# Kernel optimization log

Hardware: AMD Instinct MI355X
Metric: run time of the kernel (lower is better)

Reference implementation:

```python
import jax, jax.numpy as jnp
import numpy as np

S, B, TD = 1024, 2, 138
D, H, Dh, L, F = 1024, 16, 64, 8, 2048
EPS = 1e-5


def setup_inputs() -> dict:
    key = jax.random.key(0)
    ks = jax.random.split(key, 32)
    std = 0.02

    def w(k, shape):
        return (jax.random.normal(k, shape, jnp.float32) * std)

    return {
        'tokens': jax.random.normal(ks[0], (S, B, TD), jnp.float32),
        'Win': w(ks[1], (D, TD)), 'bin_': jnp.zeros((D,), jnp.float32),
        'pos_emb': w(ks[2], (S, D)),
        'Wq': w(ks[3], (L, D, D)), 'bq': jnp.zeros((L, D), jnp.float32),
        'Wk': w(ks[4], (L, D, D)), 'bk': jnp.zeros((L, D), jnp.float32),
        'Wv': w(ks[5], (L, D, D)), 'bv': jnp.zeros((L, D), jnp.float32),
        'Wo': w(ks[6], (L, D, D)), 'bo': jnp.zeros((L, D), jnp.float32),
        'W1': w(ks[7], (L, F, D)), 'b1': jnp.zeros((L, F), jnp.float32),
        'W2': w(ks[8], (L, D, F)), 'b2': jnp.zeros((L, D), jnp.float32),
        'g1': jnp.ones((L, D), jnp.float32), 'be1': jnp.zeros((L, D), jnp.float32),
        'g2': jnp.ones((L, D), jnp.float32), 'be2': jnp.zeros((L, D), jnp.float32),
        'Wh': w(ks[9], (1, D)), 'bh': jnp.zeros((1,), jnp.float32),
    }


def _ln(x, g, b):
    mu = jnp.mean(x, axis=-1, keepdims=True)
    var = jnp.mean(jnp.square(x - mu), axis=-1, keepdims=True)
    return (x - mu) * jax.lax.rsqrt(var + EPS) * g + b


def _rope_tables(seq_len):
    inv_freq = 1.0 / (10000.0 ** (jnp.arange(0, Dh, 2, dtype=jnp.float32) / Dh))
    ang = jnp.arange(seq_len, dtype=jnp.float32)[:, None] * inv_freq  # (S, Dh/2)
    cos = jnp.repeat(jnp.cos(ang), 2, axis=-1)  # (S, Dh) interleaved
    sin = jnp.repeat(jnp.sin(ang), 2, axis=-1)
    return cos, sin


def _apply_rope(x, cos, sin):
    # x: (B, H, S, Dh); rotate_every_two: pairs (x0, x1) -> (-x1, x0)
    rot = jnp.stack([-x[..., 1::2], x[..., 0::2]], axis=-1).reshape(x.shape)
    return x * cos + rot * sin


def reference(tokens, Win, bin_, pos_emb, Wq, bq, Wk, bk, Wv, bv, Wo, bo,
              W1, b1, W2, b2, g1, be1, g2, be2, Wh, bh):
    s = tokens.shape[0]
    x = jnp.einsum('sbt,dt->sbd', tokens, Win) + bin_ + pos_emb[:s, None, :]
    cos, sin = _rope_tables(s)
    causal = jnp.tril(jnp.ones((s, s), dtype=bool))
    scale = 1.0 / np.sqrt(Dh)

    def to_heads(y):  # (S,B,D) -> (B,H,S,Dh)
        return jnp.transpose(y.reshape(s, -1, H, Dh), (1, 2, 0, 3))

    def layer(x, p):
        wq, bq_, wk, bk_, wv, bv_, wo, bo_, w1, b1_, w2, b2_, g1_, be1_, g2_, be2_ = p
        qh = _apply_rope(to_heads(jnp.einsum('sbd,ed->sbe', x, wq) + bq_), cos, sin)
        kh = _apply_rope(to_heads(jnp.einsum('sbd,ed->sbe', x, wk) + bk_), cos, sin)
        vh = to_heads(jnp.einsum('sbd,ed->sbe', x, wv) + bv_)
        scores = jnp.einsum('bhqd,bhkd->bhqk', qh, kh) * scale
        scores = jnp.where(causal, scores, -jnp.inf)
        attn = jax.nn.softmax(scores, axis=-1)
        o = jnp.einsum('bhqk,bhkd->bhqd', attn, vh)  # (B,H,S,Dh)
        o = jnp.transpose(o, (2, 0, 1, 3)).reshape(s, -1, D)
        attn_out = jnp.einsum('sbd,ed->sbe', o, wo) + bo_
        src2 = _ln(x + attn_out, g1_, be1_)
        ff = jnp.einsum('sbf,df->sbd', jax.nn.relu(jnp.einsum('sbd,fd->sbf', src2, w1) + b1_), w2) + b2_
        return _ln(src2 + ff, g2_, be2_), None

    params = (Wq, bq, Wk, bk, Wv, bv, Wo, bo, W1, b1, W2, b2, g1, be1, g2, be2)
    x, _ = jax.lax.scan(layer, x, params)
    return jnp.einsum('sbd,od->sbo', x, Wh) + bh  # (S, B, 1)
```

## Files before the change

### kernel.cpp

```cpp
#include <hip/hip_runtime.h>
#include <hip/hip_bf16.h>

typedef __hip_bfloat16 bf16;
typedef float f32x4 __attribute__((ext_vector_type(4)));
typedef float f32x16 __attribute__((ext_vector_type(16)));
typedef short s16x8 __attribute__((ext_vector_type(8)));
typedef int i32x4 __attribute__((ext_vector_type(4)));

#define S_LEN 1024
#define BATCH 2
#define TDIM 138
#define KPAD 160
#define DMOD 1024
#define NHEAD 16
#define DHEAD 64
#define NLAYER 8
#define FDIM 2048
#define MROWS 2048
static const size_t DD_ = (size_t)DMOD * DMOD;
static const size_t FD_ = (size_t)FDIM * DMOD;

__device__ __forceinline__ void load_lds16(const bf16* g, bf16* l) {
  __builtin_amdgcn_global_load_lds((const __attribute__((address_space(1))) void*)g,
                                   (__attribute__((address_space(3))) void*)l, 16, 0, 0);
}

__device__ __forceinline__ unsigned pack2(float a, float b) {
  unsigned x = __builtin_bit_cast(unsigned short, __float2bfloat16(a));
  unsigned y = __builtin_bit_cast(unsigned short, __float2bfloat16(b));
  return x | (y << 16);
}

__device__ __forceinline__ int chunk_start(int c) {
  return c == 0 ? 0 : (c == 1 ? 32 : (c == 2 ? 56 : 72));
}

__global__ __launch_bounds__(256) void f2b_layer(
    const float4* __restrict__ Wq, const float4* __restrict__ Wk,
    const float4* __restrict__ Wv, const float4* __restrict__ Wo,
    const float4* __restrict__ W1, const float4* __restrict__ W2,
    ushort4* __restrict__ dst) {
  int i = blockIdx.x * 256 + threadIdx.x;
  const int DD4 = (int)(DD_ / 4), FD4 = (int)(FD_ / 4);
  if (i >= 4 * DD4 + 2 * FD4) return;
  const float4* src; int off;
  if (i < 3 * DD4) { int w = i / DD4; off = i - w * DD4; src = w == 0 ? Wq : (w == 1 ? Wk : Wv); }
  else if (i < 4 * DD4) { src = Wo; off = i - 3 * DD4; }
  else if (i < 4 * DD4 + FD4) { src = W1; off = i - 4 * DD4; }
  else { src = W2; off = i - 4 * DD4 - FD4; }
  float4 v = src[off];
  ushort4 o;
  o.x = __builtin_bit_cast(unsigned short, __float2bfloat16(v.x));
  o.y = __builtin_bit_cast(unsigned short, __float2bfloat16(v.y));
  o.z = __builtin_bit_cast(unsigned short, __float2bfloat16(v.z));
  o.w = __builtin_bit_cast(unsigned short, __float2bfloat16(v.w));
  dst[i] = o;
}

__global__ __launch_bounds__(256) void pad_cvt(const float* __restrict__ in,
                                               bf16* __restrict__ out, int R) {
  int i = blockIdx.x * 256 + threadIdx.x;
  if (i >= R * KPAD) return;
  int r = i / KPAD, t = i - r * KPAD;
  out[i] = __float2bfloat16(t < TDIM ? in[r * TDIM + t] : 0.0f);
}

__global__ __launch_bounds__(256) void rope_table(float2* __restrict__ t) {
  int idx = blockIdx.x * 256 + threadIdx.x;
  if (idx >= S_LEN * 32) return;
  int s = idx >> 5, i = idx & 31;
  float freq = __expf(-(float)i * (2.0f / (float)DHEAD) * 9.210340371976184f);
  float sn, cs;
  sincosf((float)s * freq, &sn, &cs);
  t[idx] = make_float2(cs, sn);
}

template<int TN, int EPI>
__global__ __launch_bounds__(256) void gemm128(
    const bf16* __restrict__ A, const bf16* __restrict__ W,
    const float* __restrict__ b0p, const float* __restrict__ b1p, const float* __restrict__ b2p,
    const float2* __restrict__ rope2, float* __restrict__ Cf,
    bf16* __restrict__ Cb0, bf16* __restrict__ Cb1, bf16* __restrict__ Cb2,
    int N, int K, int nbx) {
  constexpr int NJ = TN / 32;
  constexpr int ASZ = 128 * 32, BSZ = TN * 32;
  __shared__ bf16 As[2 * ASZ];
  __shared__ bf16 Bs[2 * BSZ];
  int nwg = gridDim.x, bid = blockIdx.x;
  int wg = (bid & 7) * (nwg >> 3) + (bid >> 3);
  int bx = wg % nbx, by = wg / nbx;
  int bn = bx * TN, bm = by * 128;
  int tid = threadIdx.x, lane = tid & 63, w = tid >> 6;
  int lo = lane & 15, hi = lane >> 4;
  int wr = (w >> 1) * 64, wc = (w & 1) * (TN / 2);
  f32x4 acc[4][NJ] = {};

  int srow = tid >> 2, sseg = tid & 3;
  const bf16* gA = A + (size_t)(bm + srow) * K + sseg * 8;
  const bf16* gB = W + (size_t)(bn + srow) * K + sseg * 8;
  bf16* lA0 = As + srow * 32 + sseg * 8;
  bf16* lB0 = Bs + srow * 32 + sseg * 8;

  auto STAGE = [&](int k0, int b) {
    load_lds16(gA + k0, lA0 + b * ASZ);
    load_lds16(gA + (size_t)64 * K + k0, lA0 + b * ASZ + 64 * 32);
    load_lds16(gB + k0, lB0 + b * BSZ);
    if constexpr (TN == 128) load_lds16(gB + (size_t)64 * K + k0, lB0 + b * BSZ + 64 * 32);
  };

  int nt = K / 32;
  STAGE(0, 0);
  __syncthreads();
  int cur = 0;
  for (int t = 0; t < nt; t++) {
    if (t + 1 < nt) STAGE((t + 1) * 32, cur ^ 1);
    const bf16* Ab = As + cur * ASZ;
    const bf16* Bb = Bs + cur * BSZ;
    s16x8 af[4], bfr[NJ];
#pragma unroll
    for (int mi = 0; mi < 4; mi++) af[mi] = *(const s16x8*)(Ab + (wr + mi * 16 + lo) * 32 + hi * 8);
#pragma unroll
    for (int nj = 0; nj < NJ; nj++) bfr[nj] = *(const s16x8*)(Bb + (wc + nj * 16 + lo) * 32 + hi * 8);
#pragma unroll
    for (int mi = 0; mi < 4; mi++)
#pragma unroll
      for (int nj = 0; nj < NJ; nj++)
        acc[mi][nj] = __builtin_amdgcn_mfma_f32_16x16x32_bf16(af[mi], bfr[nj], acc[mi][nj], 0, 0, 0);
    __syncthreads();
    cur ^= 1;
  }

#pragma unroll
  for (int mi = 0; mi < 4; mi++)
#pragma unroll
    for (int nj = 0; nj < NJ; nj++)
#pragma unroll
      for (int r = 0; r < 4; r++) {
        int m = bm + wr + mi * 16 + hi * 4 + r;
        int n = bn + wc + nj * 16 + lo;
        float v = acc[mi][nj][r];
        if constexpr (EPI == 0) {
          int which = n >> 10;
          int d = n & 1023, h = d >> 6, dh = d & 63;
          int s = m >> 1, bb = m & 1;
          const float* bp = which == 0 ? b0p : (which == 1 ? b1p : b2p);
          v += bp[d];
          if (which < 2) {
            float pv = __shfl_xor(v, 1);
            float2 cn = rope2[s * 32 + (dh >> 1)];
            float o = (dh & 1) ? (v * cn.x + pv * cn.y) : (v * cn.x - pv * cn.y);
            bf16* dst = which == 0 ? Cb0 : Cb1;
            dst[(((size_t)(bb * NHEAD + h)) * S_LEN + s) * DHEAD + dh] = __float2bfloat16(o);
          } else {
            Cb2[(((size_t)(bb * NHEAD + h)) * DHEAD + dh) * S_LEN + s] = __float2bfloat16(v);
          }
        } else if constexpr (EPI == 1) {
          Cf[(size_t)m * N + n] = v + b0p[n];
        } else if constexpr (EPI == 2) {
          Cb0[(size_t)m * N + n] = __float2bfloat16(fmaxf(v + b0p[n], 0.0f));
        } else {
          float v2 = v + b0p[n] + b1p[(size_t)(m >> 1) * DMOD + n];
          Cf[(size_t)m * N + n] = v2;
          Cb0[(size_t)m * N + n] = __float2bfloat16(v2);
        }
      }
}

__global__ __launch_bounds__(256) void flash_part(const bf16* __restrict__ Q,
    const bf16* __restrict__ K, const bf16* __restrict__ Vt,
    float* __restrict__ pO, float* __restrict__ pML) {
  int bid = blockIdx.x;
  int xcd = bid & 7, idx = bid >> 3;
  int bh = xcd * 4 + idx / 20;
  int w = threadIdx.x >> 6, lane = threadIdx.x & 63;
  int widx = (idx % 20) * 4 + w;
  int c = widx < 32 ? 0 : (widx < 56 ? 1 : (widx < 72 ? 2 : 3));
  int qt = widx - chunk_start(c) + 8 * c;
  int l31 = lane & 31, hi1 = lane >> 5;
  int q0 = qt * 32, kc0 = c * 256;
  int kend = min(kc0 + 256, q0 + 32);
  int nkt = (kend - kc0 + 31) >> 5;

  const size_t qkb = (size_t)bh * S_LEN * DHEAD;
  const bf16* qp = Q + qkb + (size_t)(q0 + l31) * DHEAD + hi1 * 8;
  s16x8 bq0 = *(const s16x8*)(qp);
  s16x8 bq1 = *(const s16x8*)(qp + 16);
  s16x8 bq2 = *(const s16x8*)(qp + 32);
  s16x8 bq3 = *(const s16x8*)(qp + 48);
  const bf16* kB = K + qkb;
  const bf16* vB = Vt + qkb;
  f32x16 accO0 = {}, accO1 = {};
  float mv = -INFINITY, lv = 0.0f;
  const float SC = 0.18033688011112042f;

  auto loadTile = [&](int kc, s16x8& k0, s16x8& k1, s16x8& k2, s16x8& k3,
                      s16x8& v0, s16x8& v1, s16x8& v2, s16x8& v3) {
    const bf16* kp = kB + (size_t)(kc + l31) * DHEAD + hi1 * 8;
    k0 = *(const s16x8*)(kp);
    k1 = *(const s16x8*)(kp + 16);
    k2 = *(const s16x8*)(kp + 32);
    k3 = *(const s16x8*)(kp + 48);
    const bf16* vp = vB + (size_t)l31 * S_LEN + kc + hi1 * 8;
    v0 = *(const s16x8*)(vp);
    v1 = *(const s16x8*)(vp + 16);
    v2 = *(const s16x8*)(vp + (size_t)32 * S_LEN);
    v3 = *(const s16x8*)(vp + (size_t)32 * S_LEN + 16);
  };

  auto computeTile = [&](int kc, s16x8 ka0, s16x8 ka1, s16x8 ka2, s16x8 ka3,
                         s16x8 va00, s16x8 va01, s16x8 va10, s16x8 va11) {
    f32x16 st = {};
    st = __builtin_amdgcn_mfma_f32_32x32x16_bf16(ka0, bq0, st, 0, 0, 0);
    st = __builtin_amdgcn_mfma_f32_32x32x16_bf16(ka1, bq1, st, 0, 0, 0);
    st = __builtin_amdgcn_mfma_f32_32x32x16_bf16(ka2, bq2, st, 0, 0, 0);
    st = __builtin_amdgcn_mfma_f32_32x32x16_bf16(ka3, bq3, st, 0, 0, 0);

    bool diag = (kc >= q0);
    float pmax = -INFINITY;
#pragma unroll
    for (int j = 0; j < 16; j++) {
      float s = st[j] * SC;
      if (diag) {
        int krow = kc + (j & 3) + 8 * (j >> 2) + 4 * hi1;
        if (krow > q0 + l31) s = -INFINITY;
      }
      st[j] = s;
      pmax = fmaxf(pmax, s);
    }
    pmax = fmaxf(pmax, __shfl_xor(pmax, 32));
    float mnew = fmaxf(mv, pmax);
    float fs = exp2f(mv - mnew);
    float sum = 0.0f;
#pragma unroll
    for (int j = 0; j < 16; j++) {
      float e = exp2f(st[j] - mnew);
      st[j] = e;
      sum += e;
    }
    sum += __shfl_xor(sum, 32);
    lv = lv * fs + sum;
    mv = mnew;
    accO0 = accO0 * fs;
    accO1 = accO1 * fs;

    unsigned w0 = pack2(st[0], st[1]),   w1 = pack2(st[2], st[3]);
    unsigned w2 = pack2(st[4], st[5]),   w3 = pack2(st[6], st[7]);
    unsigned w4 = pack2(st[8], st[9]),   w5 = pack2(st[10], st[11]);
    unsigned w6 = pack2(st[12], st[13]), w7 = pack2(st[14], st[15]);
    unsigned xw0 = (unsigned)__shfl_xor((int)w0, 32), xw1 = (unsigned)__shfl_xor((int)w1, 32);
    unsigned xw2 = (unsigned)__shfl_xor((int)w2, 32), xw3 = (unsigned)__shfl_xor((int)w3, 32);
    unsigned xw4 = (unsigned)__shfl_xor((int)w4, 32), xw5 = (unsigned)__shfl_xor((int)w5, 32);
    unsigned xw6 = (unsigned)__shfl_xor((int)w6, 32), xw7 = (unsigned)__shfl_xor((int)w7, 32);
    bool hb = (hi1 != 0);
    i32x4 f0, f1;
    f0.x = (int)(hb ? xw2 : w0); f0.y = (int)(hb ? xw3 : w1);
    f0.z = (int)(hb ? w2 : xw0); f0.w = (int)(hb ? w3 : xw1);
    f1.x = (int)(hb ? xw6 : w4); f1.y = (int)(hb ? xw7 : w5);
    f1.z = (int)(hb ? w6 : xw4); f1.w = (int)(hb ? w7 : xw5);
    s16x8 pf0 = __builtin_bit_cast(s16x8, f0);
    s16x8 pf1 = __builtin_bit_cast(s16x8, f1);
    accO0 = __builtin_amdgcn_mfma_f32_32x32x16_bf16(va00, pf0, accO0, 0, 0, 0);
    accO0 = __builtin_amdgcn_mfma_f32_32x32x16_bf16(va01, pf1, accO0, 0, 0, 0);
    accO1 = __builtin_amdgcn_mfma_f32_32x32x16_bf16(va10, pf0, accO1, 0, 0, 0);
    accO1 = __builtin_amdgcn_mfma_f32_32x32x16_bf16(va11, pf1, accO1, 0, 0, 0);
  };

  s16x8 A0, A1, A2, A3, A4, A5, A6, A7;
  s16x8 B0, B1, B2, B3, B4, B5, B6, B7;
  loadTile(kc0, A0, A1, A2, A3, A4, A5, A6, A7);
  for (int kt = 0; kt < nkt; kt += 2) {
    if (kt + 1 < nkt) loadTile(kc0 + (kt + 1) * 32, B0, B1, B2, B3, B4, B5, B6, B7);
    computeTile(kc0 + kt * 32, A0, A1, A2, A3, A4, A5, A6, A7);
    if (kt + 1 < nkt) {
      if (kt + 2 < nkt) loadTile(kc0 + (kt + 2) * 32, A0, A1, A2, A3, A4, A5, A6, A7);
      computeTile(kc0 + (kt + 1) * 32, B0, B1, B2, B3, B4, B5, B6, B7);
    }
  }

  int pbase = bh * 80 + widx;
  float* po = pO + (size_t)pbase * 2048 + l31 * 64 + 4 * hi1;
#pragma unroll
  for (int jj = 0; jj < 4; jj++) {
    f32x4 v0 = {accO0[4 * jj], accO0[4 * jj + 1], accO0[4 * jj + 2], accO0[4 * jj + 3]};
    f32x4 v1 = {accO1[4 * jj], accO1[4 * jj + 1], accO1[4 * jj + 2], accO1[4 * jj + 3]};
    *(f32x4*)(po + 8 * jj) = v0;
    *(f32x4*)(po + 32 + 8 * jj) = v1;
  }
  if (hi1 == 0) {
    pML[pbase * 64 + l31] = mv;
    pML[pbase * 64 + 32 + l31] = lv;
  }
}

__global__ __launch_bounds__(256) void flash_merge(const float* __restrict__ pO,
    const float* __restrict__ pML, bf16* __restrict__ O) {
  int bid = blockIdx.x;
  int xcd = bid & 7, idx = bid >> 3;
  int bh = xcd * 4 + idx / 32, qt = idx % 32;
  int b = bh >> 4, h = bh & 15;
  int nch = (qt >> 3) + 1;
  int t = threadIdx.x;
  int dh = t & 63, r0 = t >> 6;
  int ibase = bh * 80;
#pragma unroll
  for (int j = 0; j < 8; j++) {
    int row = j * 4 + r0;
    float ms = -INFINITY;
    for (int cc = 0; cc < nch; cc++) {
      int wi = chunk_start(cc) + qt - 8 * cc;
      ms = fmaxf(ms, pML[(ibase + wi) * 64 + row]);
    }
    float l = 0.0f, o = 0.0f;
    for (int cc = 0; cc < nch; cc++) {
      int wi = chunk_start(cc) + qt - 8 * cc;
      float wgt = exp2f(pML[(ibase + wi) * 64 + row] - ms);
      l += wgt * pML[(ibase + wi) * 64 + 32 + row];
      o += wgt * pO[(size_t)(ibase + wi) * 2048 + row * 64 + dh];
    }
    int q = qt * 32 + row;
    O[((size_t)q * BATCH + b) * DMOD + h * DHEAD + dh] = __float2bfloat16(o / l);
  }
}

__global__ __launch_bounds__(256) void ln_kernel(const float* __restrict__ a,
    const float* __restrict__ r, const float* __restrict__ g,
    const float* __restrict__ be, float* __restrict__ outf, bf16* __restrict__ outb) {
  int m = blockIdx.x;
  int tid = threadIdx.x;
  float vals[4];
  float s1 = 0.f, s2 = 0.f;
  for (int j = 0; j < 4; j++) {
    int d = tid + j * 256;
    float v = a[(size_t)m * DMOD + d] + r[(size_t)m * DMOD + d];
    vals[j] = v; s1 += v; s2 += v * v;
  }
  __shared__ float red[8];
  for (int d = 1; d < 64; d <<= 1) { s1 += __shfl_xor(s1, d); s2 += __shfl_xor(s2, d); }
  int w = tid >> 6, lane = tid & 63;
  if (lane == 0) { red[w] = s1; red[4 + w] = s2; }
  __syncthreads();
  s1 = red[0] + red[1] + red[2] + red[3];
  s2 = red[4] + red[5] + red[6] + red[7];
  float mean = s1 * (1.0f / DMOD);
  float var = s2 * (1.0f / DMOD) - mean * mean;
  float rstd = rsqrtf(var + 1e-5f);
  for (int j = 0; j < 4; j++) {
    int d = tid + j * 256;
    float o = (vals[j] - mean) * rstd * g[d] + be[d];
    outf[(size_t)m * DMOD + d] = o;
    outb[(size_t)m * DMOD + d] = __float2bfloat16(o);
  }
}

__global__ __launch_bounds__(256) void head_kernel(const float* __restrict__ x,
    const float* __restrict__ Wh, const float* __restrict__ bh, float* __restrict__ out) {
  int m = blockIdx.x * 4 + (threadIdx.x >> 6);
  int lane = threadIdx.x & 63;
  float s = 0.f;
  for (int j = 0; j < 16; j++) {
    int d = lane + j * 64;
    s += x[(size_t)m * DMOD + d] * Wh[d];
  }
  for (int d = 1; d < 64; d <<= 1) s += __shfl_xor(s, d);
  if (lane == 0) out[m] = s + bh[0];
}

extern "C" void kernel_launch(void* const* d_in, const int* in_sizes, int n_in,
                              void* d_out, int out_size, void* d_ws, size_t ws_size,
                              hipStream_t stream) {
  (void)in_sizes; (void)n_in; (void)out_size; (void)ws_size;
  const float* tokens = (const float*)d_in[0];
  const float* Win    = (const float*)d_in[1];
  const float* binp   = (const float*)d_in[2];
  const float* pos    = (const float*)d_in[3];
  const float* Wq     = (const float*)d_in[4];
  const float* bq     = (const float*)d_in[5];
  const float* Wk     = (const float*)d_in[6];
  const float* bk     = (const float*)d_in[7];
  const float* Wv     = (const float*)d_in[8];
  const float* bv     = (const float*)d_in[9];
  const float* Wo     = (const float*)d_in[10];
  const float* bo     = (const float*)d_in[11];
  const float* W1     = (const float*)d_in[12];
  const float* b1     = (const float*)d_in[13];
  const float* W2     = (const float*)d_in[14];
  const float* b2     = (const float*)d_in[15];
  const float* g1     = (const float*)d_in[16];
  const float* be1    = (const float*)d_in[17];
  const float* g2     = (const float*)d_in[18];
  const float* be2    = (const float*)d_in[19];
  const float* Wh     = (const float*)d_in[20];
  const float* bhp    = (const float*)d_in[21];
  float* out = (float*)d_out;

  char* p = (char*)d_ws;
  auto alloc = [&](size_t bytes) { char* r = p; p += (bytes + 255) & ~(size_t)255; return r; };
  float* xf   = (float*)alloc((size_t)MROWS * DMOD * 4);
  bf16*  xb   = (bf16*) alloc((size_t)MROWS * DMOD * 2);
  float* x2f  = (float*)alloc((size_t)MROWS * DMOD * 4);
  bf16*  x2b  = (bf16*) alloc((size_t)MROWS * DMOD * 2);
  float* tmpf = (float*)alloc((size_t)MROWS * DMOD * 4);
  bf16*  qb   = (bf16*) alloc((size_t)MROWS * DMOD * 2);
  bf16*  kb   = (bf16*) alloc((size_t)MROWS * DMOD * 2);
  bf16*  vt   = (bf16*) alloc((size_t)MROWS * DMOD * 2);
  bf16*  ob   = (bf16*) alloc((size_t)MROWS * DMOD * 2);
  bf16*  hb   = (bf16*) alloc((size_t)MROWS * FDIM * 2);
  bf16*  wb   = (bf16*) alloc((4 * DD_ + 2 * FD_) * 2);
  bf16*  tokb = (bf16*) alloc((size_t)MROWS * KPAD * 2);
  bf16*  winb = (bf16*) alloc((size_t)DMOD * KPAD * 2);
  float2* rope2 = (float2*)alloc((size_t)S_LEN * 32 * 8);
  float* pO   = (float*)alloc((size_t)32 * 80 * 2048 * 4);
  float* pML  = (float*)alloc((size_t)32 * 80 * 64 * 4);

  rope_table<<<(S_LEN * 32 + 255) / 256, 256, 0, stream>>>(rope2);
  pad_cvt<<<(MROWS * KPAD + 255) / 256, 256, 0, stream>>>(tokens, tokb, MROWS);
  pad_cvt<<<(DMOD * KPAD + 255) / 256, 256, 0, stream>>>(Win, winb, DMOD);
  gemm128<128, 3><<<128, 256, 0, stream>>>(
      tokb, winb, binp, pos, nullptr, nullptr,
      xf, xb, nullptr, nullptr, DMOD, KPAD, 8);

  const int nW4 = (int)((4 * DD_ + 2 * FD_) / 4);

  for (int l = 0; l < NLAYER; l++) {
    f2b_layer<<<(nW4 + 255) / 256, 256, 0, stream>>>(
        (const float4*)(Wq + l * DD_), (const float4*)(Wk + l * DD_),
        (const float4*)(Wv + l * DD_), (const float4*)(Wo + l * DD_),
        (const float4*)(W1 + l * FD_), (const float4*)(W2 + l * FD_), (ushort4*)wb);

    gemm128<128, 0><<<384, 256, 0, stream>>>(
        xb, wb, bq + l * DMOD, bk + l * DMOD, bv + l * DMOD, rope2,
        nullptr, qb, kb, vt, 3 * DMOD, DMOD, 24);

    flash_part<<<640, 256, 0, stream>>>(qb, kb, vt, pO, pML);
    flash_merge<<<1024, 256, 0, stream>>>(pO, pML, ob);

    gemm128<64, 1><<<256, 256, 0, stream>>>(
        ob, wb + 3 * DD_, bo + l * DMOD, nullptr, nullptr, nullptr,
        tmpf, nullptr, nullptr, nullptr, DMOD, DMOD, 16);

    ln_kernel<<<MROWS, 256, 0, stream>>>(xf, tmpf, g1 + l * DMOD, be1 + l * DMOD, x2f, x2b);

    gemm128<128, 2><<<256, 256, 0, stream>>>(
        x2b, wb + 4 * DD_, b1 + l * FDIM, nullptr, nullptr, nullptr,
        nullptr, hb, nullptr, nullptr, FDIM, DMOD, 16);

    gemm128<64, 1><<<256, 256, 0, stream>>>(
        hb, wb + 4 * DD_ + FD_, b2 + l * DMOD, nullptr, nullptr, nullptr,
        tmpf, nullptr, nullptr, nullptr, DMOD, FDIM, 16);

    ln_kernel<<<MROWS, 256, 0, stream>>>(x2f, tmpf, g2 + l * DMOD, be2 + l * DMOD, xf, xb);
  }

  head_kernel<<<MROWS / 4, 256, 0, stream>>>(xf, Wh, bhp, out);
}
```

Baseline: 1.598 ms.

## Use 64x128 GEMM tiles with split-K for N=1024 projections, reduced in LayerNorm

Replaces the 128xTN GEMM tile with a 64x128 tile, doubling the workgroup count for every projection so more of the GPU's compute units stay busy. The Wo and W2 GEMMs (N=1024) also split K in two, writing two partial fp32 buffers that the LayerNorm kernel sums along with the residual. This targets underutilisation from the low workgroup counts of the previous launches. In exchange it adds extra fp32 partial writes and reads plus lower per-tile data reuse.

```diff
diff --git a/kernel.cpp b/kernel.cpp
--- a/kernel.cpp
+++ b/kernel.cpp
@@ -75,40 +75,42 @@
   t[idx] = make_float2(cs, sn);
 }
 
-template<int TN, int EPI>
-__global__ __launch_bounds__(256) void gemm128(
+template<int EPI, int SPLITK>
+__global__ __launch_bounds__(256) void gemm64(
     const bf16* __restrict__ A, const bf16* __restrict__ W,
     const float* __restrict__ b0p, const float* __restrict__ b1p, const float* __restrict__ b2p,
     const float2* __restrict__ rope2, float* __restrict__ Cf,
     bf16* __restrict__ Cb0, bf16* __restrict__ Cb1, bf16* __restrict__ Cb2,
-    int N, int K, int nbx) {
-  constexpr int NJ = TN / 32;
-  constexpr int ASZ = 128 * 32, BSZ = TN * 32;
+    int N, int K, int nby) {
+  constexpr int ASZ = 64 * 32, BSZ = 128 * 32;
   __shared__ bf16 As[2 * ASZ];
   __shared__ bf16 Bs[2 * BSZ];
   int nwg = gridDim.x, bid = blockIdx.x;
   int wg = (bid & 7) * (nwg >> 3) + (bid >> 3);
-  int bx = wg % nbx, by = wg / nbx;
-  int bn = bx * TN, bm = by * 128;
+  int nbx = N >> 7;
+  int by = wg % nby, bx2 = wg / nby;
+  int kh = 0, bx = bx2;
+  if constexpr (SPLITK == 2) { bx = bx2 % nbx; kh = bx2 / nbx; }
+  int bn = bx * 128, bm = by * 64;
+  int Kh = K / SPLITK, koff = kh * Kh;
   int tid = threadIdx.x, lane = tid & 63, w = tid >> 6;
   int lo = lane & 15, hi = lane >> 4;
-  int wr = (w >> 1) * 64, wc = (w & 1) * (TN / 2);
-  f32x4 acc[4][NJ] = {};
-
-  int srow = tid >> 2, sseg = tid & 3;
-  const bf16* gA = A + (size_t)(bm + srow) * K + sseg * 8;
-  const bf16* gB = W + (size_t)(bn + srow) * K + sseg * 8;
-  bf16* lA0 = As + srow * 32 + sseg * 8;
-  bf16* lB0 = Bs + srow * 32 + sseg * 8;
+  int wr = (w >> 1) * 32, wc = (w & 1) * 64;
+  f32x4 acc[2][4] = {};
+
+  int srow = tid >> 2, sseg = (tid & 3) * 8;
+  const bf16* gA = A + (size_t)(bm + srow) * K + koff + sseg;
+  const bf16* gB = W + (size_t)(bn + srow) * K + koff + sseg;
+  bf16* lA = As + srow * 32 + sseg;
+  bf16* lB = Bs + srow * 32 + sseg;
 
   auto STAGE = [&](int k0, int b) {
-    load_lds16(gA + k0, lA0 + b * ASZ);
-    load_lds16(gA + (size_t)64 * K + k0, lA0 + b * ASZ + 64 * 32);
-    load_lds16(gB + k0, lB0 + b * BSZ);
-    if constexpr (TN == 128) load_lds16(gB + (size_t)64 * K + k0, lB0 + b * BSZ + 64 * 32);
+    load_lds16(gA + k0, lA + b * ASZ);
+    load_lds16(gB + k0, lB + b * BSZ);
+    load_lds16(gB + (size_t)64 * K + k0, lB + b * BSZ + 64 * 32);
   };
 
-  int nt = K / 32;
+  int nt = Kh / 32;
   STAGE(0, 0);
   __syncthreads();
   int cur = 0;
@@ -116,24 +118,24 @@
     if (t + 1 < nt) STAGE((t + 1) * 32, cur ^ 1);
     const bf16* Ab = As + cur * ASZ;
     const bf16* Bb = Bs + cur * BSZ;
-    s16x8 af[4], bfr[NJ];
-#pragma unroll
-    for (int mi = 0; mi < 4; mi++) af[mi] = *(const s16x8*)(Ab + (wr + mi * 16 + lo) * 32 + hi * 8);
-#pragma unroll
-    for (int nj = 0; nj < NJ; nj++) bfr[nj] = *(const s16x8*)(Bb + (wc + nj * 16 + lo) * 32 + hi * 8);
-#pragma unroll
-    for (int mi = 0; mi < 4; mi++)
-#pragma unroll
-      for (int nj = 0; nj < NJ; nj++)
+    s16x8 af[2], bfr[4];
+#pragma unroll
+    for (int mi = 0; mi < 2; mi++) af[mi] = *(const s16x8*)(Ab + (wr + mi * 16 + lo) * 32 + hi * 8);
+#pragma unroll
+    for (int nj = 0; nj < 4; nj++) bfr[nj] = *(const s16x8*)(Bb + (wc + nj * 16 + lo) * 32 + hi * 8);
+#pragma unroll
+    for (int mi = 0; mi < 2; mi++)
+#pragma unroll
+      for (int nj = 0; nj < 4; nj++)
         acc[mi][nj] = __builtin_amdgcn_mfma_f32_16x16x32_bf16(af[mi], bfr[nj], acc[mi][nj], 0, 0, 0);
     __syncthreads();
     cur ^= 1;
   }
 
 #pragma unroll
-  for (int mi = 0; mi < 4; mi++)
-#pragma unroll
-    for (int nj = 0; nj < NJ; nj++)
+  for (int mi = 0; mi < 2; mi++)
+#pragma unroll
+    for (int nj = 0; nj < 4; nj++)
 #pragma unroll
       for (int r = 0; r < 4; r++) {
         int m = bm + wr + mi * 16 + hi * 4 + r;
@@ -155,7 +157,8 @@
             Cb2[(((size_t)(bb * NHEAD + h)) * DHEAD + dh) * S_LEN + s] = __float2bfloat16(v);
           }
         } else if constexpr (EPI == 1) {
-          Cf[(size_t)m * N + n] = v + b0p[n];
+          if (SPLITK == 1 || kh == 0) v += b0p[n];
+          Cf[((size_t)kh * MROWS + m) * N + n] = v;
         } else if constexpr (EPI == 2) {
           Cb0[(size_t)m * N + n] = __float2bfloat16(fmaxf(v + b0p[n], 0.0f));
         } else {
@@ -323,15 +326,17 @@
 }
 
 __global__ __launch_bounds__(256) void ln_kernel(const float* __restrict__ a,
-    const float* __restrict__ r, const float* __restrict__ g,
-    const float* __restrict__ be, float* __restrict__ outf, bf16* __restrict__ outb) {
+    const float* __restrict__ r0, const float* __restrict__ r1,
+    const float* __restrict__ g, const float* __restrict__ be,
+    float* __restrict__ outf, bf16* __restrict__ outb) {
   int m = blockIdx.x;
   int tid = threadIdx.x;
   float vals[4];
   float s1 = 0.f, s2 = 0.f;
   for (int j = 0; j < 4; j++) {
     int d = tid + j * 256;
-    float v = a[(size_t)m * DMOD + d] + r[(size_t)m * DMOD + d];
+    size_t i = (size_t)m * DMOD + d;
+    float v = a[i] + r0[i] + r1[i];
     vals[j] = v; s1 += v; s2 += v * v;
   }
   __shared__ float red[8];
@@ -399,7 +404,7 @@
   bf16*  xb   = (bf16*) alloc((size_t)MROWS * DMOD * 2);
   float* x2f  = (float*)alloc((size_t)MROWS * DMOD * 4);
   bf16*  x2b  = (bf16*) alloc((size_t)MROWS * DMOD * 2);
-  float* tmpf = (float*)alloc((size_t)MROWS * DMOD * 4);
+  float* tmpf = (float*)alloc((size_t)2 * MROWS * DMOD * 4);
   bf16*  qb   = (bf16*) alloc((size_t)MROWS * DMOD * 2);
   bf16*  kb   = (bf16*) alloc((size_t)MROWS * DMOD * 2);
   bf16*  vt   = (bf16*) alloc((size_t)MROWS * DMOD * 2);
@@ -415,9 +420,9 @@
   rope_table<<<(S_LEN * 32 + 255) / 256, 256, 0, stream>>>(rope2);
   pad_cvt<<<(MROWS * KPAD + 255) / 256, 256, 0, stream>>>(tokens, tokb, MROWS);
   pad_cvt<<<(DMOD * KPAD + 255) / 256, 256, 0, stream>>>(Win, winb, DMOD);
-  gemm128<128, 3><<<128, 256, 0, stream>>>(
+  gemm64<3, 1><<<256, 256, 0, stream>>>(
       tokb, winb, binp, pos, nullptr, nullptr,
-      xf, xb, nullptr, nullptr, DMOD, KPAD, 8);
+      xf, xb, nullptr, nullptr, DMOD, KPAD, 32);
 
   const int nW4 = (int)((4 * DD_ + 2 * FD_) / 4);
 
@@ -427,28 +432,30 @@
         (const float4*)(Wv + l * DD_), (const float4*)(Wo + l * DD_),
         (const float4*)(W1 + l * FD_), (const float4*)(W2 + l * FD_), (ushort4*)wb);
 
-    gemm128<128, 0><<<384, 256, 0, stream>>>(
+    gemm64<0, 1><<<768, 256, 0, stream>>>(
         xb, wb, bq + l * DMOD, bk + l * DMOD, bv + l * DMOD, rope2,
-        nullptr, qb, kb, vt, 3 * DMOD, DMOD, 24);
+        nullptr, qb, kb, vt, 3 * DMOD, DMOD, 32);
 
     flash_part<<<640, 256, 0, stream>>>(qb, kb, vt, pO, pML);
     flash_merge<<<1024, 256, 0, stream>>>(pO, pML, ob);
 
-    gemm128<64, 1><<<256, 256, 0, stream>>>(
+    gemm64<1, 2><<<512, 256, 0, stream>>>(
         ob, wb + 3 * DD_, bo + l * DMOD, nullptr, nullptr, nullptr,
-        tmpf, nullptr, nullptr, nullptr, DMOD, DMOD, 16);
-
-    ln_kernel<<<MROWS, 256, 0, stream>>>(xf, tmpf, g1 + l * DMOD, be1 + l * DMOD, x2f, x2b);
-
-    gemm128<128, 2><<<256, 256, 0, stream>>>(
+        tmpf, nullptr, nullptr, nullptr, DMOD, DMOD, 32);
+
+    ln_kernel<<<MROWS, 256, 0, stream>>>(xf, tmpf, tmpf + (size_t)MROWS * DMOD,
+                                         g1 + l * DMOD, be1 + l * DMOD, x2f, x2b);
+
+    gemm64<2, 1><<<512, 256, 0, stream>>>(
         x2b, wb + 4 * DD_, b1 + l * FDIM, nullptr, nullptr, nullptr,
-        nullptr, hb, nullptr, nullptr, FDIM, DMOD, 16);
-
-    gemm128<64, 1><<<256, 256, 0, stream>>>(
+        nullptr, hb, nullptr, nullptr, FDIM, DMOD, 32);
+
+    gemm64<1, 2><<<512, 256, 0, stream>>>(
         hb, wb + 4 * DD_ + FD_, b2 + l * DMOD, nullptr, nullptr, nullptr,
-        tmpf, nullptr, nullptr, nullptr, DMOD, FDIM, 16);
-
-    ln_kernel<<<MROWS, 256, 0, stream>>>(x2f, tmpf, g2 + l * DMOD, be2 + l * DMOD, xf, xb);
+        tmpf, nullptr, nullptr, nullptr, DMOD, FDIM, 32);
+
+    ln_kernel<<<MROWS, 256, 0, stream>>>(x2f, tmpf, tmpf + (size_t)MROWS * DMOD,
+                                         g2 + l * DMOD, be2 + l * DMOD, xf, xb);
   }
 
   head_kernel<<<MROWS / 4, 256, 0, stream>>>(xf, Wh, bhp, out);
```

Result: faster. 1.457 ms (-8.8%).
